# Kernel tuning notes

Measured on AMD Instinct MI355X. Metric: run time of the kernel, lower is better.

The kernel has to match this reference:

```python
import jax, jax.numpy as jnp
import numpy as np

S = 7
NUM_CLASSES = 20
BATCH = 16384


def _iou(a, b):
    # a, b: [..., 4] boxes in (cx, cy, w, h) format
    ax1, ay1 = a[..., 0] - a[..., 2] / 2, a[..., 1] - a[..., 3] / 2
    ax2, ay2 = a[..., 0] + a[..., 2] / 2, a[..., 1] + a[..., 3] / 2
    bx1, by1 = b[..., 0] - b[..., 2] / 2, b[..., 1] - b[..., 3] / 2
    bx2, by2 = b[..., 0] + b[..., 2] / 2, b[..., 1] + b[..., 3] / 2
    iw = jnp.clip(jnp.minimum(ax2, bx2) - jnp.maximum(ax1, bx1), 0.0)
    ih = jnp.clip(jnp.minimum(ay2, by2) - jnp.maximum(ay1, by1), 0.0)
    inter = iw * ih
    union = a[..., 2] * a[..., 3] + b[..., 2] * b[..., 3] - inter
    return inter / (union + 1e-10)


def setup_inputs() -> dict:
    key = jax.random.key(0)
    k1, k2, k3, k4 = jax.random.split(key, 4)
    preds = jax.random.uniform(k1, (BATCH, S, S, 30), jnp.float32, 0.05, 0.95)
    box = jax.random.uniform(k2, (BATCH, S, S, 4), jnp.float32, 0.05, 0.95)
    conf = jax.random.bernoulli(k3, 0.3, (BATCH, S, S, 1)).astype(jnp.float32)
    cls = jax.random.uniform(k4, (BATCH, S, S, NUM_CLASSES), jnp.float32)
    labels = jnp.concatenate([box, conf, box, conf, cls], axis=-1)
    return {"preds": preds, "labels": labels}


def reference(preds, labels):
    obj = labels[..., 4] == 1.0          # [N, S, S] responsible-cell mask
    obj_f = obj.astype(preds.dtype)
    noobj_f = 1.0 - obj_f

    iou1 = _iou(preds[..., 0:4], labels[..., 0:4])
    iou2 = _iou(preds[..., 5:9], labels[..., 0:4])
    b1 = iou1 > iou2                      # box 1 is responsible
    b1f = b1.astype(preds.dtype)[..., None]

    # responsible / other box slices selected per cell
    p_xy = b1f * preds[..., 0:2] + (1 - b1f) * preds[..., 5:7]
    l_xy = b1f * labels[..., 0:2] + (1 - b1f) * labels[..., 5:7]
    p_wh = b1f * preds[..., 2:4] + (1 - b1f) * preds[..., 7:9]
    l_wh = b1f * labels[..., 2:4] + (1 - b1f) * labels[..., 7:9]
    conf_resp = jnp.where(b1, preds[..., 4], preds[..., 9])
    conf_other = jnp.where(b1, preds[..., 9], preds[..., 4])
    iou_resp = jnp.where(b1, iou1, iou2)
    iou_other = jnp.where(b1, iou2, iou1)

    loss_xy = 5.0 * jnp.sum(obj_f * jnp.sum((p_xy - l_xy) ** 2, axis=-1))
    loss_wh = jnp.sum(obj_f * jnp.sum((jnp.sqrt(p_wh) - jnp.sqrt(l_wh)) ** 2, axis=-1))
    loss_obj = jnp.sum(obj_f * (conf_resp - iou_resp) ** 2)
    loss_noobj_in = 0.5 * jnp.sum(obj_f * (conf_other - iou_other) ** 2)
    loss_noobj_out = 0.5 * jnp.sum(noobj_f * (preds[..., 4] ** 2 + preds[..., 9] ** 2))
    loss_cls = jnp.sum(obj_f * jnp.sum((preds[..., 10:] - labels[..., 10:]) ** 2, axis=-1))

    total = loss_xy + loss_wh + loss_obj + loss_noobj_in + loss_noobj_out + loss_cls
    return total / preds.shape[0]
```

## Files before the change

kernel.cpp:

```cpp
#include <hip/hip_runtime.h>

#define S 7
#define NUM_CLASSES 20
#define BATCH 16384
#define NCELLS (BATCH * S * S)
#define BLOCK 256
#define CPB   256
#define TILE_FLOATS (CPB * 30)
#define TILE_F4     (TILE_FLOATS / 4)

__device__ __forceinline__ void async_load16(const float* g, float* s) {
    __builtin_amdgcn_global_load_lds(
        (const __attribute__((address_space(1))) void*)g,
        (__attribute__((address_space(3))) void*)s,
        16, 0, 0);
}

__device__ __forceinline__ float iou_f(float acx, float acy, float aw, float ah,
                                       float bcx, float bcy, float bw, float bh) {
    float ax1 = acx - aw * 0.5f, ay1 = acy - ah * 0.5f;
    float ax2 = acx + aw * 0.5f, ay2 = acy + ah * 0.5f;
    float bx1 = bcx - bw * 0.5f, by1 = bcy - bh * 0.5f;
    float bx2 = bcx + bw * 0.5f, by2 = bcy + bh * 0.5f;
    float iw = fminf(ax2, bx2) - fmaxf(ax1, bx1);
    iw = fmaxf(iw, 0.0f);
    float ih = fminf(ay2, by2) - fmaxf(ay1, by1);
    ih = fmaxf(ih, 0.0f);
    float inter = iw * ih;
    float uni = aw * ah + bw * bh - inter;
    return inter / (uni + 1e-10f);
}

__global__ __launch_bounds__(BLOCK) void yolo_loss_kernel(
        const float* __restrict__ preds,
        const float* __restrict__ labels,
        float* __restrict__ out) {
    __shared__ float sp[TILE_FLOATS];
    __shared__ float sl[TILE_FLOATS];

    const float* gp = preds  + (size_t)blockIdx.x * TILE_FLOATS;
    const float* gl = labels + (size_t)blockIdx.x * TILE_FLOATS;

#pragma unroll
    for (int it = 0; it < 8; ++it) {
        int i = (threadIdx.x + it * BLOCK) * 4;
        if (i < TILE_FLOATS) {
            async_load16(gp + i, sp + i);
            async_load16(gl + i, sl + i);
        }
    }
    __syncthreads();

    float p[30], l[30];
    const float2* pp = (const float2*)(sp + threadIdx.x * 30);
    const float2* ll = (const float2*)(sl + threadIdx.x * 30);
#pragma unroll
    for (int j = 0; j < 15; ++j) {
        float2 v = pp[j];
        p[2 * j] = v.x; p[2 * j + 1] = v.y;
        float2 w = ll[j];
        l[2 * j] = w.x; l[2 * j + 1] = w.y;
    }

    float obj = (l[4] == 1.0f) ? 1.0f : 0.0f;

    float iou1 = iou_f(p[0], p[1], p[2], p[3], l[0], l[1], l[2], l[3]);
    float iou2 = iou_f(p[5], p[6], p[7], p[8], l[0], l[1], l[2], l[3]);
    bool b1 = iou1 > iou2;

    float pxy0 = b1 ? p[0] : p[5];
    float pxy1 = b1 ? p[1] : p[6];
    float pwh0 = b1 ? p[2] : p[7];
    float pwh1 = b1 ? p[3] : p[8];
    float conf_resp  = b1 ? p[4] : p[9];
    float conf_other = b1 ? p[9] : p[4];
    float iou_resp   = b1 ? iou1 : iou2;
    float iou_other  = b1 ? iou2 : iou1;

    float dx = pxy0 - l[0];
    float dy = pxy1 - l[1];
    float loss_xy = dx * dx + dy * dy;

    float sw0 = sqrtf(pwh0) - sqrtf(l[2]);
    float sw1 = sqrtf(pwh1) - sqrtf(l[3]);
    float loss_wh = sw0 * sw0 + sw1 * sw1;

    float d_obj = conf_resp - iou_resp;
    float loss_obj = d_obj * d_obj;

    float d_no = conf_other - iou_other;
    float loss_noobj_in = 0.5f * d_no * d_no;

    float loss_noobj_out = 0.5f * (1.0f - obj) * (p[4] * p[4] + p[9] * p[9]);

    float loss_cls = 0.0f;
#pragma unroll
    for (int c = 10; c < 30; ++c) {
        float d = p[c] - l[c];
        loss_cls += d * d;
    }

    float loss = obj * (5.0f * loss_xy + loss_wh + loss_obj + loss_noobj_in + loss_cls)
               + loss_noobj_out;

#pragma unroll
    for (int off = 32; off > 0; off >>= 1)
        loss += __shfl_down(loss, off, 64);

    __shared__ float wsum[BLOCK / 64];
    int lane = threadIdx.x & 63;
    int wid  = threadIdx.x >> 6;
    if (lane == 0) wsum[wid] = loss;
    __syncthreads();
    if (threadIdx.x == 0) {
        float s = wsum[0] + wsum[1] + wsum[2] + wsum[3];
        atomicAdd(out, s * (1.0f / (float)BATCH));
    }
}

extern "C" void kernel_launch(void* const* d_in, const int* in_sizes, int n_in,
                              void* d_out, int out_size, void* d_ws, size_t ws_size,
                              hipStream_t stream) {
    const float* preds  = (const float*)d_in[0];
    const float* labels = (const float*)d_in[1];
    float* out = (float*)d_out;

    hipMemsetAsync(out, 0, sizeof(float), stream);

    int nblocks = NCELLS / CPB;
    yolo_loss_kernel<<<nblocks, BLOCK, 0, stream>>>(preds, labels, out);
}
```

Measured before the change: 203.7 us.

## Use persistent single-wave blocks with double-buffered async LDS tile loads

Replaces the one-tile-per-256-thread-block launch with 512 persistent 64-thread blocks. Each block loops over 128-cell tiles and prefetches the next tile into a second LDS buffer while it computes the current one. Each lane handles two cells per tile and accumulates locally, so there is one atomic per block and no block-level barrier. The cost is far less parallelism (512 waves on a large GPU) and a hand-written vmcnt wait that must match the number of outstanding loads.

```diff
diff --git a/kernel.cpp b/kernel.cpp
--- a/kernel.cpp
+++ b/kernel.cpp
@@ -4,10 +4,12 @@
 #define NUM_CLASSES 20
 #define BATCH 16384
 #define NCELLS (BATCH * S * S)
-#define BLOCK 256
-#define CPB   256
+#define CPB 128
+#define NTILES (NCELLS / CPB)
+#define BLOCK 64
+#define GRID 512
 #define TILE_FLOATS (CPB * 30)
-#define TILE_F4     (TILE_FLOATS / 4)
+#define GPL 15
 
 __device__ __forceinline__ void async_load16(const float* g, float* s) {
     __builtin_amdgcn_global_load_lds(
@@ -31,29 +33,10 @@
     return inter / (uni + 1e-10f);
 }
 
-__global__ __launch_bounds__(BLOCK) void yolo_loss_kernel(
-        const float* __restrict__ preds,
-        const float* __restrict__ labels,
-        float* __restrict__ out) {
-    __shared__ float sp[TILE_FLOATS];
-    __shared__ float sl[TILE_FLOATS];
-
-    const float* gp = preds  + (size_t)blockIdx.x * TILE_FLOATS;
-    const float* gl = labels + (size_t)blockIdx.x * TILE_FLOATS;
-
-#pragma unroll
-    for (int it = 0; it < 8; ++it) {
-        int i = (threadIdx.x + it * BLOCK) * 4;
-        if (i < TILE_FLOATS) {
-            async_load16(gp + i, sp + i);
-            async_load16(gl + i, sl + i);
-        }
-    }
-    __syncthreads();
-
+__device__ __forceinline__ float cell_loss(const float* cp, const float* cl) {
     float p[30], l[30];
-    const float2* pp = (const float2*)(sp + threadIdx.x * 30);
-    const float2* ll = (const float2*)(sl + threadIdx.x * 30);
+    const float2* pp = (const float2*)cp;
+    const float2* ll = (const float2*)cl;
 #pragma unroll
     for (int j = 0; j < 15; ++j) {
         float2 v = pp[j];
@@ -100,22 +83,67 @@
         loss_cls += d * d;
     }
 
-    float loss = obj * (5.0f * loss_xy + loss_wh + loss_obj + loss_noobj_in + loss_cls)
-               + loss_noobj_out;
+    return obj * (5.0f * loss_xy + loss_wh + loss_obj + loss_noobj_in + loss_cls)
+         + loss_noobj_out;
+}
+
+__global__ __launch_bounds__(BLOCK) void yolo_loss_kernel(
+        const float* __restrict__ preds,
+        const float* __restrict__ labels,
+        float* __restrict__ out) {
+    __shared__ __align__(16) float sp[2][TILE_FLOATS];
+    __shared__ __align__(16) float sl[2][TILE_FLOATS];
+
+    const int lane = threadIdx.x;
+    float acc = 0.0f;
+
+    const int f0 = lane * 4;
+
+    int t = blockIdx.x;
+    const int iters = (NTILES - (int)blockIdx.x + GRID - 1) / GRID;
+
+    {
+        const float* gp = preds  + (size_t)t * TILE_FLOATS;
+        const float* gl = labels + (size_t)t * TILE_FLOATS;
+#pragma unroll
+        for (int it = 0; it < GPL; ++it) {
+            int f = f0 + it * 256;
+            async_load16(gp + f, &sp[0][f]);
+            async_load16(gl + f, &sl[0][f]);
+        }
+    }
+
+    int bb = 0;
+    for (int i = 1; i < iters; ++i) {
+        const int tn = t + GRID;
+        const float* gp = preds  + (size_t)tn * TILE_FLOATS;
+        const float* gl = labels + (size_t)tn * TILE_FLOATS;
+#pragma unroll
+        for (int it = 0; it < GPL; ++it) {
+            int f = f0 + it * 256;
+            async_load16(gp + f, &sp[bb ^ 1][f]);
+            async_load16(gl + f, &sl[bb ^ 1][f]);
+        }
+        asm volatile("s_waitcnt vmcnt(30)" ::: "memory");
+        __builtin_amdgcn_sched_barrier(0);
+
+        acc += cell_loss(&sp[bb][lane * 30],        &sl[bb][lane * 30]);
+        acc += cell_loss(&sp[bb][(lane + 64) * 30], &sl[bb][(lane + 64) * 30]);
+
+        t = tn;
+        bb ^= 1;
+    }
+
+    asm volatile("s_waitcnt vmcnt(0)" ::: "memory");
+    __builtin_amdgcn_sched_barrier(0);
+    acc += cell_loss(&sp[bb][lane * 30],        &sl[bb][lane * 30]);
+    acc += cell_loss(&sp[bb][(lane + 64) * 30], &sl[bb][(lane + 64) * 30]);
 
 #pragma unroll
     for (int off = 32; off > 0; off >>= 1)
-        loss += __shfl_down(loss, off, 64);
-
-    __shared__ float wsum[BLOCK / 64];
-    int lane = threadIdx.x & 63;
-    int wid  = threadIdx.x >> 6;
-    if (lane == 0) wsum[wid] = loss;
-    __syncthreads();
-    if (threadIdx.x == 0) {
-        float s = wsum[0] + wsum[1] + wsum[2] + wsum[3];
-        atomicAdd(out, s * (1.0f / (float)BATCH));
-    }
+        acc += __shfl_down(acc, off, 64);
+    if (lane == 0)
+        atomicAdd(out, acc * (1.0f / (float)BATCH));
 }
 
 extern "C" void kernel_launch(void* const* d_in, const int* in_sizes, int n_in,
@@ -127,6 +155,5 @@
 
     hipMemsetAsync(out, 0, sizeof(float), stream);
 
-    int nblocks = NCELLS / CPB;
-    yolo_loss_kernel<<<nblocks, BLOCK, 0, stream>>>(preds, labels, out);
+    yolo_loss_kernel<<<GRID, BLOCK, 0, stream>>>(preds, labels, out);
 }
```

Result: slower. 208.8 us (+2.5%).

## Load cells directly from global memory, skip unused label fields and LDS staging

Applied to the files above, without the earlier changes.

Drops the LDS staging via global_load_lds and has each thread read its own cell straight from global memory as float2 loads. Label fields 6-9 (the duplicate box copy) are never loaded, which cuts label read traffic. The block-level shared-memory reduction is replaced by one atomicAdd per wavefront. Uncoalesced per-thread strided loads (120-byte stride) may use cache lines less efficiently than the cooperative tile load, and four times as many atomics hit one address.

```diff
diff --git a/kernel.cpp b/kernel.cpp
--- a/kernel.cpp
+++ b/kernel.cpp
@@ -5,16 +5,7 @@
 #define BATCH 16384
 #define NCELLS (BATCH * S * S)
 #define BLOCK 256
-#define CPB   256
-#define TILE_FLOATS (CPB * 30)
-#define TILE_F4     (TILE_FLOATS / 4)
-
-__device__ __forceinline__ void async_load16(const float* g, float* s) {
-    __builtin_amdgcn_global_load_lds(
-        (const __attribute__((address_space(1))) void*)g,
-        (__attribute__((address_space(3))) void*)s,
-        16, 0, 0);
-}
+#define GRID (NCELLS / BLOCK)
 
 __device__ __forceinline__ float iou_f(float acx, float acy, float aw, float ah,
                                        float bcx, float bcy, float bw, float bh) {
@@ -35,37 +26,31 @@
         const float* __restrict__ preds,
         const float* __restrict__ labels,
         float* __restrict__ out) {
-    __shared__ float sp[TILE_FLOATS];
-    __shared__ float sl[TILE_FLOATS];
+    const int cell = blockIdx.x * BLOCK + threadIdx.x;
 
-    const float* gp = preds  + (size_t)blockIdx.x * TILE_FLOATS;
-    const float* gl = labels + (size_t)blockIdx.x * TILE_FLOATS;
+    const float2* pp = (const float2*)(preds  + (size_t)cell * 30);
+    const float2* lp = (const float2*)(labels + (size_t)cell * 30);
 
+    float2 P[15];
 #pragma unroll
-    for (int it = 0; it < 8; ++it) {
-        int i = (threadIdx.x + it * BLOCK) * 4;
-        if (i < TILE_FLOATS) {
-            async_load16(gp + i, sp + i);
-            async_load16(gl + i, sl + i);
-        }
-    }
-    __syncthreads();
+    for (int j = 0; j < 15; ++j) P[j] = pp[j];
 
-    float p[30], l[30];
-    const float2* pp = (const float2*)(sp + threadIdx.x * 30);
-    const float2* ll = (const float2*)(sl + threadIdx.x * 30);
+    float2 L0 = lp[0];
+    float2 L1 = lp[1];
+    float2 L2 = lp[2];
+    float2 LC[10];
 #pragma unroll
-    for (int j = 0; j < 15; ++j) {
-        float2 v = pp[j];
-        p[2 * j] = v.x; p[2 * j + 1] = v.y;
-        float2 w = ll[j];
-        l[2 * j] = w.x; l[2 * j + 1] = w.y;
-    }
+    for (int j = 0; j < 10; ++j) LC[j] = lp[5 + j];
 
-    float obj = (l[4] == 1.0f) ? 1.0f : 0.0f;
+    float p[30];
+#pragma unroll
+    for (int j = 0; j < 15; ++j) { p[2 * j] = P[j].x; p[2 * j + 1] = P[j].y; }
+    const float lx = L0.x, ly = L0.y, lw = L1.x, lh = L1.y, lconf = L2.x;
 
-    float iou1 = iou_f(p[0], p[1], p[2], p[3], l[0], l[1], l[2], l[3]);
-    float iou2 = iou_f(p[5], p[6], p[7], p[8], l[0], l[1], l[2], l[3]);
+    float obj = (lconf == 1.0f) ? 1.0f : 0.0f;
+
+    float iou1 = iou_f(p[0], p[1], p[2], p[3], lx, ly, lw, lh);
+    float iou2 = iou_f(p[5], p[6], p[7], p[8], lx, ly, lw, lh);
     bool b1 = iou1 > iou2;
 
     float pxy0 = b1 ? p[0] : p[5];
@@ -77,12 +62,12 @@
     float iou_resp   = b1 ? iou1 : iou2;
     float iou_other  = b1 ? iou2 : iou1;
 
-    float dx = pxy0 - l[0];
-    float dy = pxy1 - l[1];
+    float dx = pxy0 - lx;
+    float dy = pxy1 - ly;
     float loss_xy = dx * dx + dy * dy;
 
-    float sw0 = sqrtf(pwh0) - sqrtf(l[2]);
-    float sw1 = sqrtf(pwh1) - sqrtf(l[3]);
+    float sw0 = sqrtf(pwh0) - sqrtf(lw);
+    float sw1 = sqrtf(pwh1) - sqrtf(lh);
     float loss_wh = sw0 * sw0 + sw1 * sw1;
 
     float d_obj = conf_resp - iou_resp;
@@ -95,9 +80,10 @@
 
     float loss_cls = 0.0f;
 #pragma unroll
-    for (int c = 10; c < 30; ++c) {
-        float d = p[c] - l[c];
-        loss_cls += d * d;
+    for (int j = 0; j < 10; ++j) {
+        float d0 = p[10 + 2 * j] - LC[j].x;
+        float d1 = p[11 + 2 * j] - LC[j].y;
+        loss_cls += d0 * d0 + d1 * d1;
     }
 
     float loss = obj * (5.0f * loss_xy + loss_wh + loss_obj + loss_noobj_in + loss_cls)
@@ -106,16 +92,8 @@
 #pragma unroll
     for (int off = 32; off > 0; off >>= 1)
         loss += __shfl_down(loss, off, 64);
-
-    __shared__ float wsum[BLOCK / 64];
-    int lane = threadIdx.x & 63;
-    int wid  = threadIdx.x >> 6;
-    if (lane == 0) wsum[wid] = loss;
-    __syncthreads();
-    if (threadIdx.x == 0) {
-        float s = wsum[0] + wsum[1] + wsum[2] + wsum[3];
-        atomicAdd(out, s * (1.0f / (float)BATCH));
-    }
+    if ((threadIdx.x & 63) == 0)
+        atomicAdd(out, loss * (1.0f / (float)BATCH));
 }
 
 extern "C" void kernel_launch(void* const* d_in, const int* in_sizes, int n_in,
@@ -127,6 +105,5 @@
 
     hipMemsetAsync(out, 0, sizeof(float), stream);
 
-    int nblocks = NCELLS / CPB;
-    yolo_loss_kernel<<<nblocks, BLOCK, 0, stream>>>(preds, labels, out);
+    yolo_loss_kernel<<<GRID, BLOCK, 0, stream>>>(preds, labels, out);
 }
```

New measurement: 312.9 us. 1.54x slower.
